# Kernel optimization log

Measured on AMD Instinct MI355X. Metric: run time of the kernel, lower is better.

The kernel has to match this reference:

```python
import jax, jax.numpy as jnp
import numpy as np

N_NODES = 50000
N_EDGES = 200000
D = 384
R = 2  # num_relations


def setup_inputs() -> dict:
    key = jax.random.key(0)
    ks = jax.random.split(key, 16)
    inp = {
        "embeddings": jax.random.normal(ks[0], (N_NODES, D), dtype=jnp.float32),
        "edge_index": jax.random.randint(ks[1], (2, N_EDGES), 0, N_NODES, dtype=jnp.int64),
        "edge_type": jax.random.randint(ks[2], (N_EDGES,), 0, R, dtype=jnp.int64),
    }
    # RGCNConv params for 3 layers: per-relation weight, root weight, bias
    s = 1.0 / np.sqrt(D)
    for i, kk in zip((1, 2, 3), range(3)):
        inp[f"W{i}"] = jax.random.uniform(ks[3 + 3 * kk], (R, D, D), dtype=jnp.float32, minval=-s, maxval=s)
        inp[f"root{i}"] = jax.random.uniform(ks[4 + 3 * kk], (D, D), dtype=jnp.float32, minval=-s, maxval=s)
        inp[f"bias{i}"] = jnp.zeros((D,), dtype=jnp.float32)
    return inp


def _rgcn_conv(x, src, dst, edge_type, W, root, bias):
    # PyG RGCNConv with aggr='mean': for each relation, mean-aggregate neighbor
    # features over edges of that relation, then apply relation weight; plus
    # root transform and bias. We transform-then-aggregate (equivalent, linear).
    out = x @ root + bias
    for r in range(R):
        xr = x @ W[r]                                   # [N, D]
        mask = (edge_type == r).astype(x.dtype)         # [E]
        msg = xr[src] * mask[:, None]                   # [E, D] gather
        s = jax.ops.segment_sum(msg, dst, num_segments=N_NODES)    # [N, D]
        cnt = jax.ops.segment_sum(mask, dst, num_segments=N_NODES)  # [N]
        out = out + s / jnp.maximum(cnt, 1.0)[:, None]  # mean (0 if no edges)
    return out


def reference(embeddings, edge_index, edge_type, W1, root1, bias1, W2, root2, bias2, W3, root3, bias3):
    src, dst = edge_index[0], edge_index[1]
    x = jax.nn.relu(_rgcn_conv(embeddings, src, dst, edge_type, W1, root1, bias1))
    # dropout is identity in eval mode
    x = jax.nn.relu(_rgcn_conv(x, src, dst, edge_type, W2, root2, bias2))
    x = _rgcn_conv(x, src, dst, edge_type, W3, root3, bias3)
    return x
```

## Files before the change

### kernel.cpp

```cpp
#include <hip/hip_runtime.h>
#include <hip/hip_bf16.h>


#define D 384
#define NC 1152
#define NP 1280
#define BM 256
#define BN 256
#define BK 32
#define NKT (D / BK)
#define NTN (NP / BN)

typedef __attribute__((ext_vector_type(8))) short short8;
typedef __attribute__((ext_vector_type(4))) float floatx4;
typedef unsigned int uint;
typedef unsigned short ushort;

#define BAR() asm volatile("s_barrier" ::: "memory")
#define WAIT_LGKM0() asm volatile("s_waitcnt lgkmcnt(0)" ::: "memory")
#define WAIT_VM8() asm volatile("s_waitcnt vmcnt(8)" ::: "memory")
#define WAIT_VM4() asm volatile("s_waitcnt vmcnt(4)" ::: "memory")
#define WAIT_VM0() asm volatile("s_waitcnt vmcnt(0)" ::: "memory")

__device__ __forceinline__ void load_lds16(const void* g, void* l) {
    __builtin_amdgcn_global_load_lds(
        (const __attribute__((address_space(1))) void*)g,
        (__attribute__((address_space(3))) void*)l, 16, 0, 0);
}

__device__ __forceinline__ ushort f2bf(float x) {
    __hip_bfloat16 h = __float2bfloat16(x);
    return *reinterpret_cast<ushort*>(&h);
}

__device__ __forceinline__ uint pack2(float a, float b) {
    return (uint)f2bf(a) | ((uint)f2bf(b) << 16);
}

__device__ __forceinline__ void stage_tile(const ushort* __restrict__ g,
                                           ushort* l, int grow0, int kt,
                                           int rmax, int tid)
{
#pragma unroll
    for (int j = 0; j < 2; ++j) {
        const int ch = j * 512 + tid;
        const int row = ch >> 2;
        const int cs = ch & 3;
        const int gc = cs ^ ((row >> 1) & 3);
        const int gr = min(grow0 + row, rmax);
        load_lds16(g + (size_t)gr * D + kt * BK + gc * 8, l + (size_t)ch * 8);
    }
}

__global__ __launch_bounds__(512, 2) void gemm_bf16_mfma(
    const ushort* __restrict__ A, const ushort* __restrict__ BT,
    ushort* __restrict__ C, int M, int nwg)
{
    __shared__ alignas(16) ushort As[4][BM * BK];
    __shared__ alignas(16) ushort Bs[4][BN * BK];

    const int o = blockIdx.x;
    const int xcd = o & 7, lid = o >> 3;
    const int q = nwg >> 3, r = nwg & 7;
    const int wg = (xcd < r ? xcd * (q + 1) : r * (q + 1) + (xcd - r) * q) + lid;
    const int bnt = wg % NTN, bmt = wg / NTN;
    const int bm = bmt * BM, bn = bnt * BN;

    const int tid = threadIdx.x;
    const int wave = tid >> 6, lane = tid & 63;
    const int wr = wave >> 2, wc = wave & 3;
    const int l15 = lane & 15, k8 = lane >> 4;

    floatx4 acc[8][4] = {};

    stage_tile(A, As[0], bm, 0, M - 1, tid);
    stage_tile(BT, Bs[0], bn, 0, NP - 1, tid);
    stage_tile(A, As[1], bm, 1, M - 1, tid);
    stage_tile(BT, Bs[1], bn, 1, NP - 1, tid);
    stage_tile(A, As[2], bm, 2, M - 1, tid);
    stage_tile(BT, Bs[2], bn, 2, NP - 1, tid);
    WAIT_VM8();
    BAR();

    short8 bf[4];
    for (int j = 0; j < NKT; ++j) {
        const ushort* Ab = As[j & 3];
        const ushort* Bb = Bs[j & 3];
        const int js = j + 3;
        const int sb = js & 3;

        short8 af[4];
#pragma unroll
        for (int mi = 0; mi < 4; ++mi) {
            const int m = wr * 128 + mi * 16 + l15;
            af[mi] = *(const short8*)(Ab + m * BK + ((k8 ^ ((m >> 1) & 3)) << 3));
        }
#pragma unroll
        for (int ni = 0; ni < 4; ++ni) {
            const int n = wc * 64 + ni * 16 + l15;
            bf[ni] = *(const short8*)(Bb + n * BK + ((k8 ^ ((n >> 1) & 3)) << 3));
        }
        if (js < NKT) stage_tile(A, As[sb], bm, js, M - 1, tid);
        BAR();
        WAIT_LGKM0();
        __builtin_amdgcn_sched_barrier(0);
        __builtin_amdgcn_s_setprio(1);
#pragma unroll
        for (int mi = 0; mi < 4; ++mi)
#pragma unroll
            for (int ni = 0; ni < 4; ++ni)
                acc[mi][ni] = __builtin_amdgcn_mfma_f32_16x16x32_bf16(
                    af[mi], bf[ni], acc[mi][ni], 0, 0, 0);
        __builtin_amdgcn_s_setprio(0);
        BAR();

#pragma unroll
        for (int mi = 0; mi < 4; ++mi) {
            const int m = wr * 128 + 64 + mi * 16 + l15;
            af[mi] = *(const short8*)(Ab + m * BK + ((k8 ^ ((m >> 1) & 3)) << 3));
        }
        if (js < NKT) stage_tile(BT, Bs[sb], bn, js, NP - 1, tid);
        BAR();
        WAIT_LGKM0();
        __builtin_amdgcn_sched_barrier(0);
        __builtin_amdgcn_s_setprio(1);
#pragma unroll
        for (int mi = 0; mi < 4; ++mi)
#pragma unroll
            for (int ni = 0; ni < 4; ++ni)
                acc[4 + mi][ni] = __builtin_amdgcn_mfma_f32_16x16x32_bf16(
                    af[mi], bf[ni], acc[4 + mi][ni], 0, 0, 0);
        __builtin_amdgcn_s_setprio(0);
        if (j < NKT - 3)       { WAIT_VM8(); }
        else if (j == NKT - 3) { WAIT_VM4(); }
        else if (j == NKT - 2) { WAIT_VM0(); }
        BAR();
    }

    if (bm + BM <= M && bn + BN <= NC) {
#pragma unroll
        for (int a = 0; a < 8; ++a) {
            const int rbase = bm + wr * 128 + (a >> 2) * 64 + (a & 3) * 16 + k8 * 4;
#pragma unroll
            for (int reg = 0; reg < 4; ++reg) {
                const int row = rbase + reg;
#pragma unroll
                for (int ni = 0; ni < 4; ++ni) {
                    const int col = bn + wc * 64 + ni * 16 + l15;
                    C[(size_t)row * NC + col] = f2bf(acc[a][ni][reg]);
                }
            }
        }
    } else {
#pragma unroll
        for (int a = 0; a < 8; ++a) {
            const int rbase = bm + wr * 128 + (a >> 2) * 64 + (a & 3) * 16 + k8 * 4;
#pragma unroll
            for (int reg = 0; reg < 4; ++reg) {
                const int row = rbase + reg;
                if (row < M) {
#pragma unroll
                    for (int ni = 0; ni < 4; ++ni) {
                        const int col = bn + wc * 64 + ni * 16 + l15;
                        if (col < NC)
                            C[(size_t)row * NC + col] = f2bf(acc[a][ni][reg]);
                    }
                }
            }
        }
    }
}


__global__ __launch_bounds__(256) void count_edges(
    const int* __restrict__ dst, const int* __restrict__ et,
    int* __restrict__ cntI, int E, int M)
{
    const int e = blockIdx.x * blockDim.x + threadIdx.x;
    if (e < E) atomicAdd(&cntI[(size_t)et[e] * M + dst[e]], 1);
}

__global__ __launch_bounds__(256) void finalize_cnt(
    const int* __restrict__ cntI, float* __restrict__ invc, int n)
{
    const int i = blockIdx.x * blockDim.x + threadIdx.x;
    if (i < n) invc[i] = 1.0f / (float)max(cntI[i], 1);
}

__global__ __launch_bounds__(1024) void scan_local(
    const int* __restrict__ hist, int* __restrict__ offs,
    int* __restrict__ bsums, int n)
{
    __shared__ int tmp[1024];
    const int tid = threadIdx.x;
    const int i = blockIdx.x * 1024 + tid;
    const int v = (i < n) ? hist[i] : 0;
    tmp[tid] = v;
    __syncthreads();
#pragma unroll
    for (int off = 1; off < 1024; off <<= 1) {
        const int add = (tid >= off) ? tmp[tid - off] : 0;
        __syncthreads();
        tmp[tid] += add;
        __syncthreads();
    }
    if (i < n) offs[i] = tmp[tid] - v;
    if (tid == 1023) bsums[blockIdx.x] = tmp[1023];
}

__global__ __launch_bounds__(1024) void scan_bsums(
    int* __restrict__ bsums, int* __restrict__ total_out, int nb)
{
    __shared__ int tmp[1024];
    const int tid = threadIdx.x;
    const int v = (tid < nb) ? bsums[tid] : 0;
    tmp[tid] = v;
    __syncthreads();
#pragma unroll
    for (int off = 1; off < 1024; off <<= 1) {
        const int add = (tid >= off) ? tmp[tid - off] : 0;
        __syncthreads();
        tmp[tid] += add;
        __syncthreads();
    }
    if (tid < nb) bsums[tid] = tmp[tid] - v;
    if (tid == 1023) *total_out = tmp[1023];
}

__global__ __launch_bounds__(1024) void scan_add(
    int* __restrict__ offs, const int* __restrict__ bsums, int n)
{
    const int i = blockIdx.x * 1024 + threadIdx.x;
    if (i < n) offs[i] += bsums[blockIdx.x];
}

__global__ __launch_bounds__(256) void fill_sorted(
    const int* __restrict__ src, const int* __restrict__ dst,
    const int* __restrict__ et, const int* __restrict__ offs,
    int* __restrict__ cursor, int* __restrict__ sorted, int E, int M)
{
    const int e = blockIdx.x * blockDim.x + threadIdx.x;
    if (e < E) {
        const int key = et[e] * M + dst[e];
        const int pos = offs[key] + atomicAdd(&cursor[key], 1);
        sorted[pos] = src[e];
    }
}

__global__ __launch_bounds__(256) void build_bt(
    const float* __restrict__ root1, const float* __restrict__ W1,
    const float* __restrict__ root2, const float* __restrict__ W2,
    const float* __restrict__ root3, const float* __restrict__ W3,
    ushort* __restrict__ BT)
{
    __shared__ float tile[32][33];
    const int l = blockIdx.z;
    const float* root = (l == 0) ? root1 : (l == 1) ? root2 : root3;
    const float* W    = (l == 0) ? W1    : (l == 1) ? W2    : W3;
    const int kt = blockIdx.x * 32;
    const int nt = blockIdx.y * 32;
    const int tx = threadIdx.x & 31;
    const int ty = threadIdx.x >> 5;
    const float* srcm;
    int noff;
    if (nt < D)          { srcm = root;      noff = 0; }
    else if (nt < 2 * D) { srcm = W;         noff = D; }
    else                 { srcm = W + D * D; noff = 2 * D; }
    const int n = nt - noff + tx;
#pragma unroll
    for (int i = 0; i < 4; ++i) {
        const int k = kt + ty + i * 8;
        tile[ty + i * 8][tx] = srcm[(size_t)k * D + n];
    }
    __syncthreads();
    ushort* dst = BT + (size_t)l * NP * D;
#pragma unroll
    for (int i = 0; i < 4; ++i) {
        const int nn = nt + ty + i * 8;
        const int kk = kt + tx;
        dst[(size_t)nn * D + kk] = f2bf(tile[tx][ty + i * 8]);
    }
}

__global__ __launch_bounds__(256) void cast_f32_to_bf16(
    const float* __restrict__ x, ushort* __restrict__ y, int n4)
{
    const int i = blockIdx.x * blockDim.x + threadIdx.x;
    if (i < n4) {
        const float4 v = ((const float4*)x)[i];
        uint2 o;
        o.x = pack2(v.x, v.y);
        o.y = pack2(v.z, v.w);
        ((uint2*)y)[i] = o;
    }
}

__global__ __launch_bounds__(256) void aggregate_all(
    const ushort* __restrict__ TC, const int* __restrict__ sorted,
    const int* __restrict__ offs, const float* __restrict__ invc,
    const float* __restrict__ bias, ushort* __restrict__ outb,
    float* __restrict__ outf, int M, int relu)
{
    const int wave = threadIdx.x >> 6;
    const int lane = threadIdx.x & 63;
    const int d = blockIdx.x * 4 + wave;
    if (d >= M) return;

    float v[6];
    {
        const uint* rp = (const uint*)(TC + (size_t)d * NC);
#pragma unroll
        for (int p = 0; p < 3; ++p) {
            const uint b = rp[lane + 64 * p];
            const float2 bb = *(const float2*)(bias + (lane + 64 * p) * 2);
            v[2 * p]     = __uint_as_float(b << 16) + bb.x;
            v[2 * p + 1] = __uint_as_float(b & 0xffff0000u) + bb.y;
        }
    }
#pragma unroll
    for (int r = 0; r < 2; ++r) {
        const int key = r * M + d;
        const int beg = offs[key], end = offs[key + 1];
        float g[6] = {0.f, 0.f, 0.f, 0.f, 0.f, 0.f};
        for (int i = beg; i < end; ++i) {
            const int s = sorted[i];
            const uint* tp = (const uint*)(TC + (size_t)s * NC + D + r * D);
#pragma unroll
            for (int p = 0; p < 3; ++p) {
                const uint b = tp[lane + 64 * p];
                g[2 * p]     += __uint_as_float(b << 16);
                g[2 * p + 1] += __uint_as_float(b & 0xffff0000u);
            }
        }
        const float ic = invc[key];
#pragma unroll
        for (int j = 0; j < 6; ++j) v[j] += ic * g[j];
    }
    if (relu) {
#pragma unroll
        for (int j = 0; j < 6; ++j) v[j] = fmaxf(v[j], 0.f);
    }
    if (outb) {
        uint* op = (uint*)(outb + (size_t)d * D);
#pragma unroll
        for (int p = 0; p < 3; ++p) op[lane + 64 * p] = pack2(v[2 * p], v[2 * p + 1]);
    } else {
        float2* op = (float2*)(outf + (size_t)d * D);
#pragma unroll
        for (int p = 0; p < 3; ++p)
            op[lane + 64 * p] = make_float2(v[2 * p], v[2 * p + 1]);
    }
}

extern "C" void kernel_launch(void* const* d_in, const int* in_sizes, int n_in,
                              void* d_out, int out_size, void* d_ws, size_t ws_size,
                              hipStream_t stream)
{
    const float* emb   = (const float*)d_in[0];
    const int*   eidx  = (const int*)d_in[1];
    const int*   et    = (const int*)d_in[2];
    const float* W1    = (const float*)d_in[3];
    const float* root1 = (const float*)d_in[4];
    const float* bias1 = (const float*)d_in[5];
    const float* W2    = (const float*)d_in[6];
    const float* root2 = (const float*)d_in[7];
    const float* bias2 = (const float*)d_in[8];
    const float* W3    = (const float*)d_in[9];
    const float* root3 = (const float*)d_in[10];
    const float* bias3 = (const float*)d_in[11];

    float* out = (float*)d_out;
    const int M = in_sizes[0] / D;
    const int E = in_sizes[1] / 2;
    const int* src  = eidx;
    const int* dstv = eidx + E;

    const int n = 2 * M;
    const int nb = (n + 1023) / 1024;

    char* w = (char*)d_ws;
    ushort* TC = (ushort*)w;          w += (size_t)M * NC * 2;
    ushort* Xb = (ushort*)w;          w += (size_t)M * D * 2;
    ushort* BT = (ushort*)w;          w += (size_t)3 * NP * D * 2;
    float* invcnt = (float*)w;        w += (size_t)n * 4;
    int* cntI = (int*)w;              w += (size_t)n * 4;
    int* offs = (int*)w;              w += ((size_t)n + 1) * 4;
    int* sorted = (int*)w;            w += (size_t)E * 4;
    int* bsums = (int*)w;

    hipMemsetAsync(cntI, 0, (size_t)n * sizeof(int), stream);
    count_edges<<<(E + 255) / 256, 256, 0, stream>>>(dstv, et, cntI, E, M);
    finalize_cnt<<<(n + 255) / 256, 256, 0, stream>>>(cntI, invcnt, n);
    scan_local<<<nb, 1024, 0, stream>>>(cntI, offs, bsums, n);
    scan_bsums<<<1, 1024, 0, stream>>>(bsums, offs + n, nb);
    scan_add<<<nb, 1024, 0, stream>>>(offs, bsums, n);
    hipMemsetAsync(cntI, 0, (size_t)n * sizeof(int), stream);
    fill_sorted<<<(E + 255) / 256, 256, 0, stream>>>(src, dstv, et, offs, cntI, sorted, E, M);

    build_bt<<<dim3(D / 32, NC / 32, 3), 256, 0, stream>>>(root1, W1, root2, W2, root3, W3, BT);
    cast_f32_to_bf16<<<(M * D / 4 + 255) / 256, 256, 0, stream>>>(emb, Xb, M * D / 4);

    const int Mtiles = (M + BM - 1) / BM;
    const int nwg = Mtiles * NTN;
    const float* biases[3] = {bias1, bias2, bias3};
    for (int l = 0; l < 3; ++l) {
        gemm_bf16_mfma<<<nwg, 512, 0, stream>>>(Xb, BT + (size_t)l * NP * D, TC, M, nwg);
        const bool last = (l == 2);
        aggregate_all<<<(M + 3) / 4, 256, 0, stream>>>(
            TC, sorted, offs, invcnt, biases[l],
            last ? nullptr : Xb, last ? out : nullptr, M, last ? 0 : 1);
    }
}
```

Measured before the change: 518.6 us.

## Retile GEMM to 256x192 without N padding and vectorize bf16 stores

Shrinks the GEMM N tile from 256 to 192 so the 1152-wide output splits evenly. This drops the padded 1280-column weight layout and the wasted MFMA work on padding columns. Operand roles are swapped so each lane holds four consecutive output columns, letting the epilogue write packed 8-byte stores instead of scalar bf16 stores. The K loop becomes a single phase with one barrier per step instead of two half-steps. The cost is that the shared stage_tile still loads 256 B rows per step, so about a third of the B staging traffic is wasted.

```diff
diff --git a/kernel.cpp b/kernel.cpp
--- a/kernel.cpp
+++ b/kernel.cpp
@@ -4,12 +4,11 @@
 
 #define D 384
 #define NC 1152
-#define NP 1280
 #define BM 256
-#define BN 256
+#define BN 192
 #define BK 32
 #define NKT (D / BK)
-#define NTN (NP / BN)
+#define NTN (NC / BN)
 
 typedef __attribute__((ext_vector_type(8))) short short8;
 typedef __attribute__((ext_vector_type(4))) float floatx4;
@@ -57,7 +56,7 @@
     ushort* __restrict__ C, int M, int nwg)
 {
     __shared__ alignas(16) ushort As[4][BM * BK];
-    __shared__ alignas(16) ushort Bs[4][BN * BK];
+    __shared__ alignas(16) ushort Bs[4][BM * BK];
 
     const int o = blockIdx.x;
     const int xcd = o & 7, lid = o >> 3;
@@ -68,103 +67,86 @@
 
     const int tid = threadIdx.x;
     const int wave = tid >> 6, lane = tid & 63;
-    const int wr = wave >> 2, wc = wave & 3;
+    const int wn = wave >> 2;
+    const int wm = wave & 3;
     const int l15 = lane & 15, k8 = lane >> 4;
 
-    floatx4 acc[8][4] = {};
+    floatx4 acc[6][4] = {};
 
     stage_tile(A, As[0], bm, 0, M - 1, tid);
-    stage_tile(BT, Bs[0], bn, 0, NP - 1, tid);
+    stage_tile(BT, Bs[0], bn, 0, NC - 1, tid);
     stage_tile(A, As[1], bm, 1, M - 1, tid);
-    stage_tile(BT, Bs[1], bn, 1, NP - 1, tid);
+    stage_tile(BT, Bs[1], bn, 1, NC - 1, tid);
     stage_tile(A, As[2], bm, 2, M - 1, tid);
-    stage_tile(BT, Bs[2], bn, 2, NP - 1, tid);
+    stage_tile(BT, Bs[2], bn, 2, NC - 1, tid);
     WAIT_VM8();
     BAR();
 
-    short8 bf[4];
     for (int j = 0; j < NKT; ++j) {
         const ushort* Ab = As[j & 3];
         const ushort* Bb = Bs[j & 3];
+
+        short8 af[6], bf[4];
+#pragma unroll
+        for (int nf = 0; nf < 6; ++nf) {
+            const int rr = wn * 96 + nf * 16 + l15;
+            af[nf] = *(const short8*)(Bb + rr * BK + ((k8 ^ ((rr >> 1) & 3)) << 3));
+        }
+#pragma unroll
+        for (int mf = 0; mf < 4; ++mf) {
+            const int rr = wm * 64 + mf * 16 + l15;
+            bf[mf] = *(const short8*)(Ab + rr * BK + ((k8 ^ ((rr >> 1) & 3)) << 3));
+        }
+
         const int js = j + 3;
-        const int sb = js & 3;
-
-        short8 af[4];
-#pragma unroll
-        for (int mi = 0; mi < 4; ++mi) {
-            const int m = wr * 128 + mi * 16 + l15;
-            af[mi] = *(const short8*)(Ab + m * BK + ((k8 ^ ((m >> 1) & 3)) << 3));
-        }
-#pragma unroll
-        for (int ni = 0; ni < 4; ++ni) {
-            const int n = wc * 64 + ni * 16 + l15;
-            bf[ni] = *(const short8*)(Bb + n * BK + ((k8 ^ ((n >> 1) & 3)) << 3));
-        }
-        if (js < NKT) stage_tile(A, As[sb], bm, js, M - 1, tid);
-        BAR();
+        if (js < NKT) {
+            stage_tile(A, As[js & 3], bm, js, M - 1, tid);
+            stage_tile(BT, Bs[js & 3], bn, js, NC - 1, tid);
+        }
+
         WAIT_LGKM0();
         __builtin_amdgcn_sched_barrier(0);
         __builtin_amdgcn_s_setprio(1);
 #pragma unroll
-        for (int mi = 0; mi < 4; ++mi)
-#pragma unroll
-            for (int ni = 0; ni < 4; ++ni)
-                acc[mi][ni] = __builtin_amdgcn_mfma_f32_16x16x32_bf16(
-                    af[mi], bf[ni], acc[mi][ni], 0, 0, 0);
+        for (int nf = 0; nf < 6; ++nf)
+#pragma unroll
+            for (int mf = 0; mf < 4; ++mf)
+                acc[nf][mf] = __builtin_amdgcn_mfma_f32_16x16x32_bf16(
+                    af[nf], bf[mf], acc[nf][mf], 0, 0, 0);
         __builtin_amdgcn_s_setprio(0);
-        BAR();
-
-#pragma unroll
-        for (int mi = 0; mi < 4; ++mi) {
-            const int m = wr * 128 + 64 + mi * 16 + l15;
-            af[mi] = *(const short8*)(Ab + m * BK + ((k8 ^ ((m >> 1) & 3)) << 3));
-        }
-        if (js < NKT) stage_tile(BT, Bs[sb], bn, js, NP - 1, tid);
-        BAR();
-        WAIT_LGKM0();
-        __builtin_amdgcn_sched_barrier(0);
-        __builtin_amdgcn_s_setprio(1);
-#pragma unroll
-        for (int mi = 0; mi < 4; ++mi)
-#pragma unroll
-            for (int ni = 0; ni < 4; ++ni)
-                acc[4 + mi][ni] = __builtin_amdgcn_mfma_f32_16x16x32_bf16(
-                    af[mi], bf[ni], acc[4 + mi][ni], 0, 0, 0);
-        __builtin_amdgcn_s_setprio(0);
-        if (j < NKT - 3)       { WAIT_VM8(); }
+
+        if (j <= NKT - 4)      { WAIT_VM8(); }
         else if (j == NKT - 3) { WAIT_VM4(); }
         else if (j == NKT - 2) { WAIT_VM0(); }
         BAR();
     }
 
-    if (bm + BM <= M && bn + BN <= NC) {
-#pragma unroll
-        for (int a = 0; a < 8; ++a) {
-            const int rbase = bm + wr * 128 + (a >> 2) * 64 + (a & 3) * 16 + k8 * 4;
-#pragma unroll
-            for (int reg = 0; reg < 4; ++reg) {
-                const int row = rbase + reg;
-#pragma unroll
-                for (int ni = 0; ni < 4; ++ni) {
-                    const int col = bn + wc * 64 + ni * 16 + l15;
-                    C[(size_t)row * NC + col] = f2bf(acc[a][ni][reg]);
-                }
+    const int node0 = bm + wm * 64 + l15;
+    const int col0 = bn + wn * 96 + k8 * 4;
+    if (bm + BM <= M) {
+#pragma unroll
+        for (int mf = 0; mf < 4; ++mf) {
+            uint2* rowp = (uint2*)(C + (size_t)(node0 + mf * 16) * NC + col0);
+#pragma unroll
+            for (int nf = 0; nf < 6; ++nf) {
+                uint2 o2;
+                o2.x = pack2(acc[nf][mf][0], acc[nf][mf][1]);
+                o2.y = pack2(acc[nf][mf][2], acc[nf][mf][3]);
+                rowp[nf * 4] = o2;
             }
         }
     } else {
 #pragma unroll
-        for (int a = 0; a < 8; ++a) {
-            const int rbase = bm + wr * 128 + (a >> 2) * 64 + (a & 3) * 16 + k8 * 4;
-#pragma unroll
-            for (int reg = 0; reg < 4; ++reg) {
-                const int row = rbase + reg;
-                if (row < M) {
-#pragma unroll
-                    for (int ni = 0; ni < 4; ++ni) {
-                        const int col = bn + wc * 64 + ni * 16 + l15;
-                        if (col < NC)
-                            C[(size_t)row * NC + col] = f2bf(acc[a][ni][reg]);
-                    }
+        for (int mf = 0; mf < 4; ++mf) {
+            const int node = node0 + mf * 16;
+            if (node < M) {
+                uint2* rowp = (uint2*)(C + (size_t)node * NC + col0);
+#pragma unroll
+                for (int nf = 0; nf < 6; ++nf) {
+                    uint2 o2;
+                    o2.x = pack2(acc[nf][mf][0], acc[nf][mf][1]);
+                    o2.y = pack2(acc[nf][mf][2], acc[nf][mf][3]);
+                    rowp[nf * 4] = o2;
                 }
             }
         }
@@ -273,7 +255,7 @@
         tile[ty + i * 8][tx] = srcm[(size_t)k * D + n];
     }
     __syncthreads();
-    ushort* dst = BT + (size_t)l * NP * D;
+    ushort* dst = BT + (size_t)l * NC * D;
 #pragma unroll
     for (int i = 0; i < 4; ++i) {
         const int nn = nt + ty + i * 8;
@@ -381,7 +363,7 @@
     char* w = (char*)d_ws;
     ushort* TC = (ushort*)w;          w += (size_t)M * NC * 2;
     ushort* Xb = (ushort*)w;          w += (size_t)M * D * 2;
-    ushort* BT = (ushort*)w;          w += (size_t)3 * NP * D * 2;
+    ushort* BT = (ushort*)w;          w += (size_t)3 * NC * D * 2;
     float* invcnt = (float*)w;        w += (size_t)n * 4;
     int* cntI = (int*)w;              w += (size_t)n * 4;
     int* offs = (int*)w;              w += ((size_t)n + 1) * 4;
@@ -404,7 +386,7 @@
     const int nwg = Mtiles * NTN;
     const float* biases[3] = {bias1, bias2, bias3};
     for (int l = 0; l < 3; ++l) {
-        gemm_bf16_mfma<<<nwg, 512, 0, stream>>>(Xb, BT + (size_t)l * NP * D, TC, M, nwg);
+        gemm_bf16_mfma<<<nwg, 512, 0, stream>>>(Xb, BT + (size_t)l * NC * D, TC, M, nwg);
         const bool last = (l == 2);
         aggregate_all<<<(M + 3) / 4, 256, 0, stream>>>(
             TC, sorted, offs, invcnt, biases[l],
```

New measurement: 548.5 us. 5.8% more time.
